# Kernel tuning notes

Hardware: AMD Instinct MI355X
Metric: run time of the kernel (lower is better)

## Reference

```python
import jax, jax.numpy as jnp
import numpy as np

N = 100_000   # nodes
E = 1_600_000 # edges
F = 64        # in_feats
H = 64        # hid
EPS = 1e-5


def setup_inputs() -> dict:
    key = jax.random.key(0)
    ks = jax.random.split(key, 12)
    s = 1.0 / np.sqrt(F)
    inp = {
        "x":   jax.random.normal(ks[0], (N, F), jnp.float32),
        "src": jax.random.randint(ks[1], (E,), 0, N, jnp.int32),
        "dst": jax.random.randint(ks[2], (E,), 0, N, jnp.int32),
        # GraphConv 1: in_feats -> hid
        "W1": jax.random.uniform(ks[3], (F, H), jnp.float32, -s, s),
        "b1": jnp.zeros((H,), jnp.float32),
        "g1": jnp.ones((H,), jnp.float32),
        "be1": jnp.zeros((H,), jnp.float32),
        # GraphConv 2: hid -> hid
        "W2": jax.random.uniform(ks[4], (H, H), jnp.float32, -s, s),
        "b2": jnp.zeros((H,), jnp.float32),
        "g2": jnp.ones((H,), jnp.float32),
        "be2": jnp.zeros((H,), jnp.float32),
        # classifier hid -> 2
        "Wc": jax.random.uniform(ks[5], (H, 2), jnp.float32, -s, s),
        "bc": jnp.zeros((2,), jnp.float32),
    }
    return inp


def _graph_conv(x, src, dst, W, b):
    # DGL GraphConv, norm='both', allow_zero_in_degree=True:
    # h = D_in^{-1/2} A (D_out^{-1/2} x) W + b, degrees clamped to >= 1.
    n = x.shape[0]
    ones = jnp.ones(src.shape[0], x.dtype)
    deg_out = jnp.clip(jax.ops.segment_sum(ones, src, num_segments=n), 1.0)
    deg_in = jnp.clip(jax.ops.segment_sum(ones, dst, num_segments=n), 1.0)
    h = x * jax.lax.rsqrt(deg_out)[:, None]
    m = jax.ops.segment_sum(h[src], dst, num_segments=n)  # gather-scatter SpMM
    m = m * jax.lax.rsqrt(deg_in)[:, None]
    return m @ W + b


def _bn(h, g, be):
    # BatchNorm1d training-mode math over nodes (biased variance).
    mu = h.mean(axis=0)
    var = h.var(axis=0)
    return (h - mu) * jax.lax.rsqrt(var + EPS) * g + be


def reference(x, src, dst, W1, b1, g1, be1, W2, b2, g2, be2, Wc, bc):
    h = jax.nn.relu(_bn(_graph_conv(x, src, dst, W1, b1), g1, be1))
    # dropout is identity in eval mode
    h = jax.nn.relu(_bn(_graph_conv(h, src, dst, W2, b2), g2, be2))
    hg = h.mean(axis=0, keepdims=True)  # [1, H] graph readout
    return hg @ Wc + bc                 # [1, 2]
```

## Files before the change

### kernel.cpp

```cpp
#include <hip/hip_runtime.h>
#include <hip/hip_fp16.h>

#define FDIM 64
#define EPS 1e-5f
#define NBUCK 1024
#define LOWB 7
#define LOWMASK 127
#define RB 256
#define RT 1024
#define GRP 16
#define NSLOT 8

typedef float v2f __attribute__((ext_vector_type(2)));

__global__ void k_hist(const int* __restrict__ src, const int* __restrict__ dst,
                       int* __restrict__ histS, int* __restrict__ histD, int E, int chunk) {
    __shared__ int hs[NBUCK], hd[NBUCK];
    int tid = threadIdx.x;
    hs[tid] = 0; hd[tid] = 0;
    __syncthreads();
    int b = blockIdx.x;
    int beg = b * chunk;
    int end = min(E, beg + chunk);
    int i = beg + tid * 4;
    for (; i + 3 < end; i += RT * 4) {
        int4 s = *(const int4*)(src + i);
        int4 d = *(const int4*)(dst + i);
        atomicAdd(&hs[s.x >> LOWB], 1); atomicAdd(&hd[d.x >> LOWB], 1);
        atomicAdd(&hs[s.y >> LOWB], 1); atomicAdd(&hd[d.y >> LOWB], 1);
        atomicAdd(&hs[s.z >> LOWB], 1); atomicAdd(&hd[d.z >> LOWB], 1);
        atomicAdd(&hs[s.w >> LOWB], 1); atomicAdd(&hd[d.w >> LOWB], 1);
    }
    if (i < end) {
        for (int j = i; j < end && j < i + 4; ++j) {
            atomicAdd(&hs[src[j] >> LOWB], 1);
            atomicAdd(&hd[dst[j] >> LOWB], 1);
        }
    }
    __syncthreads();
    histS[b * NBUCK + tid] = hs[tid];
    histD[b * NBUCK + tid] = hd[tid];
}

__global__ void k_scanA(const int* __restrict__ histS, const int* __restrict__ histD,
                        int* __restrict__ psumS, int* __restrict__ psumD) {
    int bid = blockIdx.x;
    int m = bid >> 6;
    int g = (bid >> 2) & (RB / GRP - 1);
    int c = bid & 3;
    const int* hist = m ? histD : histS;
    int* psum = m ? psumD : psumS;
    int k = c * 256 + threadIdx.x;
    int s = 0;
#pragma unroll
    for (int r = 0; r < GRP; ++r)
        s += hist[(g * GRP + r) * NBUCK + k];
    psum[g * NBUCK + k] = s;
}

__global__ void k_scanB(const int* __restrict__ psumS, int* __restrict__ baseS,
                        int* __restrict__ grpbaseS,
                        const int* __restrict__ psumD, int* __restrict__ baseD,
                        int* __restrict__ grpbaseD) {
    const int* psum = blockIdx.x ? psumD : psumS;
    int* base    = blockIdx.x ? baseD : baseS;
    int* grpbase = blockIdx.x ? grpbaseD : grpbaseS;
    __shared__ int s[NBUCK];
    int k = threadIdx.x;
    int ge[RB / GRP];
    int run = 0;
#pragma unroll
    for (int g = 0; g < RB / GRP; ++g) { ge[g] = run; run += psum[g * NBUCK + k]; }
    s[k] = run;
    __syncthreads();
    for (int off = 1; off < NBUCK; off <<= 1) {
        int t = (k >= off) ? s[k - off] : 0;
        __syncthreads();
        s[k] += t;
        __syncthreads();
    }
    int excl = (k > 0) ? s[k - 1] : 0;
    base[k] = excl;
    if (k == NBUCK - 1) base[NBUCK] = s[NBUCK - 1];
#pragma unroll
    for (int g = 0; g < RB / GRP; ++g)
        grpbase[g * NBUCK + k] = excl + ge[g];
}

__global__ void k_bucket(const int* __restrict__ src, const int* __restrict__ dst,
                         const int* __restrict__ histS, const int* __restrict__ histD,
                         const int* __restrict__ grpbaseS, const int* __restrict__ grpbaseD,
                         unsigned char* __restrict__ tmpS, int* __restrict__ tmpD,
                         int E, int chunk) {
    __shared__ int curS[NBUCK], curD[NBUCK];
    int tid = threadIdx.x;
    int b = blockIdx.x;
    int g = b / GRP;
    int rs = 0, rd = 0;
    for (int r = g * GRP; r < b; ++r) {
        rs += histS[r * NBUCK + tid];
        rd += histD[r * NBUCK + tid];
    }
    curS[tid] = grpbaseS[g * NBUCK + tid] + rs;
    curD[tid] = grpbaseD[g * NBUCK + tid] + rd;
    __syncthreads();
    int beg = b * chunk;
    int end = min(E, beg + chunk);
    int i = beg + tid * 4;
    for (; i + 3 < end; i += RT * 4) {
        int4 s = *(const int4*)(src + i);
        int4 d = *(const int4*)(dst + i);
        int p;
        p = atomicAdd(&curS[s.x >> LOWB], 1); tmpS[p] = (unsigned char)(s.x & LOWMASK);
        p = atomicAdd(&curS[s.y >> LOWB], 1); tmpS[p] = (unsigned char)(s.y & LOWMASK);
        p = atomicAdd(&curS[s.z >> LOWB], 1); tmpS[p] = (unsigned char)(s.z & LOWMASK);
        p = atomicAdd(&curS[s.w >> LOWB], 1); tmpS[p] = (unsigned char)(s.w & LOWMASK);
        p = atomicAdd(&curD[d.x >> LOWB], 1); tmpD[p] = (s.x << LOWB) | (d.x & LOWMASK);
        p = atomicAdd(&curD[d.y >> LOWB], 1); tmpD[p] = (s.y << LOWB) | (d.y & LOWMASK);
        p = atomicAdd(&curD[d.z >> LOWB], 1); tmpD[p] = (s.z << LOWB) | (d.z & LOWMASK);
        p = atomicAdd(&curD[d.w >> LOWB], 1); tmpD[p] = (s.w << LOWB) | (d.w & LOWMASK);
    }
    if (i < end) {
        for (int j = i; j < end && j < i + 4; ++j) {
            int sv = src[j], dv = dst[j];
            int p = atomicAdd(&curS[sv >> LOWB], 1);
            tmpS[p] = (unsigned char)(sv & LOWMASK);
            p = atomicAdd(&curD[dv >> LOWB], 1);
            tmpD[p] = (sv << LOWB) | (dv & LOWMASK);
        }
    }
}

__global__ void k_fine(const int* __restrict__ tmpD, const int* __restrict__ baseD,
                       int* __restrict__ csr_src, int* __restrict__ rowptr,
                       const unsigned char* __restrict__ tmpS, const int* __restrict__ baseS,
                       int* __restrict__ degO, const float* __restrict__ x,
                       unsigned char* __restrict__ buf8, int N, int nbuck) {
    __shared__ int hist[128];
    __shared__ int scanv[128];
    int tid = threadIdx.x;
    if (blockIdx.x < nbuck) {
        int b = blockIdx.x;
        int s0 = baseD[b];
        int s1 = baseD[b + 1];
        if (tid < 128) hist[tid] = 0;
        __syncthreads();
        for (int i = s0 + tid; i < s1; i += 256)
            atomicAdd(&hist[tmpD[i] & LOWMASK], 1);
        __syncthreads();
        int mine = (tid < 128) ? hist[tid] : 0;
        if (tid < 128) scanv[tid] = mine;
        __syncthreads();
        for (int off = 1; off < 128; off <<= 1) {
            int t = (tid < 128 && tid >= off) ? scanv[tid - off] : 0;
            __syncthreads();
            if (tid < 128) scanv[tid] += t;
            __syncthreads();
        }
        if (tid < 128) {
            int excl = scanv[tid] - mine;
            int d = (b << LOWB) + tid;
            if (d <= N) rowptr[d] = s0 + excl;
            hist[tid] = excl;
        }
        __syncthreads();
        for (int i = s0 + tid; i < s1; i += 256) {
            int p = tmpD[i];
            int pos = atomicAdd(&hist[p & LOWMASK], 1);
            csr_src[s0 + pos] = p >> LOWB;
        }
    } else {
        int b = blockIdx.x - nbuck;
        int s0 = baseS[b];
        int s1 = baseS[b + 1];
        if (tid < 128) hist[tid] = 0;
        __syncthreads();
        for (int i = s0 + tid; i < s1; i += 256)
            atomicAdd(&hist[tmpS[i]], 1);
        __syncthreads();
        if (tid < 128) {
            int d = (b << LOWB) + tid;
            if (d < N) degO[d] = hist[tid];
        }
        int node = (b << LOWB) + (tid >> 1);
        if (node < N) {
            float rs = rsqrtf((float)max(hist[tid >> 1], 1));
            int part = tid & 1;
            const float4* xr = (const float4*)(x + (size_t)node * FDIM) + part * 8;
            int4* orow = (int4*)(buf8 + (size_t)node * FDIM + part * 32);
            int wbuf[8];
#pragma unroll
            for (int q = 0; q < 4; ++q) {
                float4 a = xr[2 * q];
                float4 c = xr[2 * q + 1];
                int t = __builtin_amdgcn_cvt_pk_fp8_f32(a.x * rs, a.y * rs, 0, false);
                t     = __builtin_amdgcn_cvt_pk_fp8_f32(a.z * rs, a.w * rs, t, true);
                wbuf[2 * q] = t;
                t = __builtin_amdgcn_cvt_pk_fp8_f32(c.x * rs, c.y * rs, 0, false);
                t = __builtin_amdgcn_cvt_pk_fp8_f32(c.z * rs, c.w * rs, t, true);
                wbuf[2 * q + 1] = t;
            }
            orow[0] = make_int4(wbuf[0], wbuf[1], wbuf[2], wbuf[3]);
            orow[1] = make_int4(wbuf[4], wbuf[5], wbuf[6], wbuf[7]);
        }
    }
}

__global__ void k_spmm8(const unsigned char* __restrict__ hin, const int* __restrict__ rowptr,
                        const int* __restrict__ csr_src, __half* __restrict__ out, int N) {
    int wid = (blockIdx.x * blockDim.x + threadIdx.x) >> 6;
    int lane = threadIdx.x & 63;
    int g = lane >> 3;
    int sl = lane & 7;
    int row = wid * 8 + g;
    bool rv = row < N;
    int start = rv ? rowptr[row] : 0;
    int end   = rv ? rowptr[row + 1] : 0;
    int deg = end - start;
    int md = deg;
    md = max(md, __shfl_xor(md, 8));
    md = max(md, __shfl_xor(md, 16));
    md = max(md, __shfl_xor(md, 32));
    float acc[8] = {0.f, 0.f, 0.f, 0.f, 0.f, 0.f, 0.f, 0.f};
    int safe = (deg > 0) ? end - 1 : 0;
    int a0 = start + sl;
    int idx_cur = csr_src[(a0 < end) ? a0 : safe];
    for (int it = 0; it < md; it += 8) {
        int idx_nxt = 0;
        if (it + 8 < md) {
            int a = start + it + 8 + sl;
            idx_nxt = csr_src[(a < end) ? a : safe];
        }
        uint2 r[8];
#pragma unroll
        for (int j = 0; j < 8; ++j) {
            int bidx = __shfl(idx_cur, (g << 3) + j);
            r[j] = ((const uint2*)(hin + ((size_t)bidx << 6)))[sl];
        }
        __builtin_amdgcn_sched_barrier(0);
#pragma unroll
        for (int j = 0; j < 8; ++j) {
            float w = (it + j < deg) ? 1.f : 0.f;
            v2f a0v = __builtin_amdgcn_cvt_pk_f32_fp8((int)r[j].x, false);
            v2f a1v = __builtin_amdgcn_cvt_pk_f32_fp8((int)r[j].x, true);
            v2f a2v = __builtin_amdgcn_cvt_pk_f32_fp8((int)r[j].y, false);
            v2f a3v = __builtin_amdgcn_cvt_pk_f32_fp8((int)r[j].y, true);
            acc[0] = fmaf(w, a0v.x, acc[0]); acc[1] = fmaf(w, a0v.y, acc[1]);
            acc[2] = fmaf(w, a1v.x, acc[2]); acc[3] = fmaf(w, a1v.y, acc[3]);
            acc[4] = fmaf(w, a2v.x, acc[4]); acc[5] = fmaf(w, a2v.y, acc[5]);
            acc[6] = fmaf(w, a3v.x, acc[6]); acc[7] = fmaf(w, a3v.y, acc[7]);
        }
        idx_cur = idx_nxt;
    }
    if (rv) {
        float rs = rsqrtf(fmaxf((float)deg, 1.0f));
        union { float4 f; __half2 h[4]; } o;
        o.h[0] = __floats2half2_rn(acc[0] * rs, acc[1] * rs);
        o.h[1] = __floats2half2_rn(acc[2] * rs, acc[3] * rs);
        o.h[2] = __floats2half2_rn(acc[4] * rs, acc[5] * rs);
        o.h[3] = __floats2half2_rn(acc[6] * rs, acc[7] * rs);
        ((float4*)(out + ((size_t)row << 6)))[sl] = o.f;
    }
}

__global__ void k_gemm_reg(const __half* __restrict__ m, const float* __restrict__ W,
                           const float* __restrict__ b, __half* __restrict__ out, int N) {
    int n = blockIdx.x * blockDim.x + threadIdx.x;
    if (n >= N) return;
    const __half2* mrow = (const __half2*)(m + (size_t)n * FDIM);
    float acc[FDIM];
#pragma unroll
    for (int j = 0; j < FDIM; ++j) acc[j] = b[j];
    for (int k0 = 0; k0 < FDIM; k0 += 8) {
        float2 f0 = __half22float2(mrow[(k0 >> 1) + 0]);
        float2 f1 = __half22float2(mrow[(k0 >> 1) + 1]);
        float2 f2 = __half22float2(mrow[(k0 >> 1) + 2]);
        float2 f3 = __half22float2(mrow[(k0 >> 1) + 3]);
        float mreg[8] = {f0.x, f0.y, f1.x, f1.y, f2.x, f2.y, f3.x, f3.y};
#pragma unroll
        for (int k1 = 0; k1 < 8; ++k1) {
            const float* Wrow = W + (k0 + k1) * FDIM;
#pragma unroll
            for (int j = 0; j < FDIM; ++j)
                acc[j] = fmaf(mreg[k1], Wrow[j], acc[j]);
        }
    }
    float4* orow = (float4*)(out + (size_t)n * FDIM);
#pragma unroll
    for (int j = 0; j < FDIM; j += 8) {
        union { __half2 h[4]; float4 f; } u;
        u.h[0] = __floats2half2_rn(acc[j + 0], acc[j + 1]);
        u.h[1] = __floats2half2_rn(acc[j + 2], acc[j + 3]);
        u.h[2] = __floats2half2_rn(acc[j + 4], acc[j + 5]);
        u.h[3] = __floats2half2_rn(acc[j + 6], acc[j + 7]);
        orow[j >> 3] = u.f;
    }
}

__global__ void k_stats_fin(const __half* __restrict__ h, float* __restrict__ ssum,
                            float* __restrict__ ssq, const float* __restrict__ g,
                            float* __restrict__ mu, float* __restrict__ coef,
                            int* __restrict__ cnt, int N) {
    __shared__ float red[4][128];
    __shared__ int lastv;
    int tid = threadIdx.x;
    int sl = tid & 7;
    int nl = tid >> 3;
    float s[8] = {0.f,0.f,0.f,0.f,0.f,0.f,0.f,0.f};
    float q[8] = {0.f,0.f,0.f,0.f,0.f,0.f,0.f,0.f};
    int stride = gridDim.x * 32;
    for (int n = blockIdx.x * 32 + nl; n < N; n += stride) {
        union { float4 f; __half2 hh[4]; } u;
        u.f = ((const float4*)(h + ((size_t)n << 6)))[sl];
#pragma unroll
        for (int p = 0; p < 4; ++p) {
            float2 v = __half22float2(u.hh[p]);
            s[2*p]   += v.x; q[2*p]   += v.x * v.x;
            s[2*p+1] += v.y; q[2*p+1] += v.y * v.y;
        }
    }
#pragma unroll
    for (int off = 8; off < 64; off <<= 1) {
#pragma unroll
        for (int p = 0; p < 8; ++p) {
            s[p] += __shfl_xor(s[p], off);
            q[p] += __shfl_xor(q[p], off);
        }
    }
    int wv = tid >> 6, lane = tid & 63;
    if (lane < 8) {
#pragma unroll
        for (int p = 0; p < 8; ++p) {
            red[wv][lane * 8 + p] = s[p];
            red[wv][64 + lane * 8 + p] = q[p];
        }
    }
    __syncthreads();
    int slot = (blockIdx.x & (NSLOT - 1)) << 6;
    if (tid < 128) {
        float v = red[0][tid] + red[1][tid] + red[2][tid] + red[3][tid];
        if (tid < 64) atomicAdd(&ssum[slot + tid], v);
        else          atomicAdd(&ssq[slot + tid - 64], v);
    }
    __syncthreads();
    if (tid == 0)
        lastv = (__hip_atomic_fetch_add(cnt, 1, __ATOMIC_ACQ_REL,
                                        __HIP_MEMORY_SCOPE_AGENT) == (int)gridDim.x - 1);
    __syncthreads();
    if (lastv && tid < 64) {
        float sv = 0.f, qv = 0.f;
#pragma unroll
        for (int p = 0; p < NSLOT; ++p) {
            sv += __hip_atomic_load(&ssum[(p << 6) + tid], __ATOMIC_RELAXED,
                                    __HIP_MEMORY_SCOPE_AGENT);
            qv += __hip_atomic_load(&ssq[(p << 6) + tid], __ATOMIC_RELAXED,
                                    __HIP_MEMORY_SCOPE_AGENT);
        }
        float m = sv / (float)N;
        float var = qv / (float)N - m * m;
        mu[tid] = m;
        coef[tid] = rsqrtf(var + EPS) * g[tid];
    }
}

__global__ void k_bnrelu_scale(const float2* __restrict__ h, const float* __restrict__ mu,
                               const float* __restrict__ coef, const float* __restrict__ be,
                               const int* __restrict__ degO, int* __restrict__ out8, int n4) {
    int i = blockIdx.x * blockDim.x + threadIdx.x;
    if (i < n4) {
        int n = i >> 4;
        int j4 = (i & 15) << 2;
        float rs = rsqrtf((float)max(degO[n], 1));
        union { __half2 hh[2]; float2 f; } u;
        u.f = h[i];
        float2 v0 = __half22float2(u.hh[0]);
        float2 v1 = __half22float2(u.hh[1]);
        float r0 = fmaxf((v0.x - mu[j4 + 0]) * coef[j4 + 0] + be[j4 + 0], 0.f) * rs;
        float r1 = fmaxf((v0.y - mu[j4 + 1]) * coef[j4 + 1] + be[j4 + 1], 0.f) * rs;
        float r2 = fmaxf((v1.x - mu[j4 + 2]) * coef[j4 + 2] + be[j4 + 2], 0.f) * rs;
        float r3 = fmaxf((v1.y - mu[j4 + 3]) * coef[j4 + 3] + be[j4 + 3], 0.f) * rs;
        int wv = __builtin_amdgcn_cvt_pk_fp8_f32(r0, r1, 0, false);
        wv     = __builtin_amdgcn_cvt_pk_fp8_f32(r2, r3, wv, true);
        out8[i] = wv;
    }
}

__global__ void k_bnmean_fin(const __half* __restrict__ h, const float* __restrict__ mu,
                             const float* __restrict__ coef, const float* __restrict__ be,
                             float* __restrict__ hsum, const float* __restrict__ Wc,
                             const float* __restrict__ bc, float* __restrict__ out,
                             int* __restrict__ cnt, int N) {
    __shared__ float red[4][64];
    __shared__ float cls[128];
    __shared__ int lastv;
    int tid = threadIdx.x;
    int sl = tid & 7;
    int nl = tid >> 3;
    int j8 = sl * 8;
    float m_[8], c_[8], b_[8];
#pragma unroll
    for (int p = 0; p < 8; ++p) { m_[p] = mu[j8 + p]; c_[p] = coef[j8 + p]; b_[p] = be[j8 + p]; }
    float s[8] = {0.f,0.f,0.f,0.f,0.f,0.f,0.f,0.f};
    int stride = gridDim.x * 32;
    for (int n = blockIdx.x * 32 + nl; n < N; n += stride) {
        union { float4 f; __half2 hh[4]; } u;
        u.f = ((const float4*)(h + ((size_t)n << 6)))[sl];
#pragma unroll
        for (int p = 0; p < 4; ++p) {
            float2 v = __half22float2(u.hh[p]);
            s[2*p]   += fmaxf((v.x - m_[2*p])   * c_[2*p]   + b_[2*p],   0.f);
            s[2*p+1] += fmaxf((v.y - m_[2*p+1]) * c_[2*p+1] + b_[2*p+1], 0.f);
        }
    }
#pragma unroll
    for (int off = 8; off < 64; off <<= 1) {
#pragma unroll
        for (int p = 0; p < 8; ++p) s[p] += __shfl_xor(s[p], off);
    }
    int wv = tid >> 6, lane = tid & 63;
    if (lane < 8) {
#pragma unroll
        for (int p = 0; p < 8; ++p) red[wv][lane * 8 + p] = s[p];
    }
    __syncthreads();
    int slot = (blockIdx.x & (NSLOT - 1)) << 6;
    if (tid < 64)
        atomicAdd(&hsum[slot + tid], red[0][tid] + red[1][tid] + red[2][tid] + red[3][tid]);
    __syncthreads();
    if (tid == 0)
        lastv = (__hip_atomic_fetch_add(cnt, 1, __ATOMIC_ACQ_REL,
                                        __HIP_MEMORY_SCOPE_AGENT) == (int)gridDim.x - 1);
    __syncthreads();
    if (lastv) {
        if (tid < 64) {
            float hg = 0.f;
#pragma unroll
            for (int p = 0; p < NSLOT; ++p)
                hg += __hip_atomic_load(&hsum[(p << 6) + tid], __ATOMIC_RELAXED,
                                        __HIP_MEMORY_SCOPE_AGENT);
            hg /= (float)N;
            cls[tid]      = hg * Wc[tid * 2 + 0];
            cls[64 + tid] = hg * Wc[tid * 2 + 1];
        }
        __syncthreads();
        if (tid == 0) {
            float a = 0.f, bv = 0.f;
            for (int k = 0; k < 64; ++k) { a += cls[k]; bv += cls[64 + k]; }
            out[0] = a + bc[0];
            out[1] = bv + bc[1];
        }
    }
}

extern "C" void kernel_launch(void* const* d_in, const int* in_sizes, int n_in,
                              void* d_out, int out_size, void* d_ws, size_t ws_size,
                              hipStream_t stream) {
    const float* x   = (const float*)d_in[0];
    const int*   src = (const int*)d_in[1];
    const int*   dst = (const int*)d_in[2];
    const float* W1  = (const float*)d_in[3];
    const float* b1  = (const float*)d_in[4];
    const float* g1  = (const float*)d_in[5];
    const float* be1 = (const float*)d_in[6];
    const float* W2  = (const float*)d_in[7];
    const float* b2  = (const float*)d_in[8];
    const float* g2  = (const float*)d_in[9];
    const float* be2 = (const float*)d_in[10];
    const float* Wc  = (const float*)d_in[11];
    const float* bc  = (const float*)d_in[12];
    float* out = (float*)d_out;

    const int N = in_sizes[0] / FDIM;
    const int E = in_sizes[1];

    char* w = (char*)d_ws;
    __half* bufA   = (__half*)w;
    __half* bufB   = bufA + (size_t)N * FDIM;
    int*   csr_src = (int*)(bufB + (size_t)N * FDIM);
    int*   degO    = csr_src + E;
    int*   rowptr  = degO + N;
    int*   histS   = rowptr + N + 2;
    int*   histD   = histS + RB * NBUCK;
    int*   baseS   = histD + RB * NBUCK;
    int*   baseD   = baseS + NBUCK + 1;
    int*   psumS   = baseD + NBUCK + 1;
    int*   psumD   = psumS + (RB / GRP) * NBUCK;
    int*   grpbaseS= psumD + (RB / GRP) * NBUCK;
    int*   grpbaseD= grpbaseS + (RB / GRP) * NBUCK;
    float* stats   = (float*)(grpbaseD + (RB / GRP) * NBUCK);
    unsigned char* tmpS = (unsigned char*)(stats + 4096);
    unsigned char* buf8 = tmpS + E;
    int*           tmpD = (int*)bufB;

    float* sum1  = stats + 0;
    float* sq1   = stats + 512;
    float* sum2  = stats + 1024;
    float* sq2   = stats + 1536;
    float* hsum  = stats + 2048;
    float* mu1   = stats + 2560;
    float* coef1 = stats + 2624;
    float* mu2   = stats + 2688;
    float* coef2 = stats + 2752;
    int*   cnt1  = (int*)(stats + 2816);
    int*   cnt2  = (int*)(stats + 2817);
    int*   cnt3  = (int*)(stats + 2818);

    const int n4 = N * (FDIM / 4);
    const int spmm8_blocks = ((N + 7) / 8 + 3) / 4;
    const int nbuck_active = (N + LOWMASK) >> LOWB;
    const int chunk = ((E + RB - 1) / RB + 3) & ~3;

    hipMemsetAsync(stats, 0, 4096 * 4, stream);

    k_hist<<<RB, RT, 0, stream>>>(src, dst, histS, histD, E, chunk);
    k_scanA<<<2 * (RB / GRP) * 4, 256, 0, stream>>>(histS, histD, psumS, psumD);
    k_scanB<<<2, NBUCK, 0, stream>>>(psumS, baseS, grpbaseS, psumD, baseD, grpbaseD);
    k_bucket<<<RB, RT, 0, stream>>>(src, dst, histS, histD, grpbaseS, grpbaseD,
                                    tmpS, tmpD, E, chunk);
    k_fine<<<2 * nbuck_active, 256, 0, stream>>>(tmpD, baseD, csr_src, rowptr,
                                                 tmpS, baseS, degO, x, buf8, N, nbuck_active);

    k_spmm8<<<spmm8_blocks, 256, 0, stream>>>(buf8, rowptr, csr_src, bufB, N);
    k_gemm_reg<<<(N + 63) / 64, 64, 0, stream>>>(bufB, W1, b1, bufA, N);
    k_stats_fin<<<256, 256, 0, stream>>>(bufA, sum1, sq1, g1, mu1, coef1, cnt1, N);
    k_bnrelu_scale<<<(n4 + 255) / 256, 256, 0, stream>>>((const float2*)bufA, mu1, coef1, be1,
                                                         degO, (int*)buf8, n4);
    k_spmm8<<<spmm8_blocks, 256, 0, stream>>>(buf8, rowptr, csr_src, bufB, N);
    k_gemm_reg<<<(N + 63) / 64, 64, 0, stream>>>(bufB, W2, b2, bufA, N);
    k_stats_fin<<<256, 256, 0, stream>>>(bufA, sum2, sq2, g2, mu2, coef2, cnt2, N);
    k_bnmean_fin<<<256, 256, 0, stream>>>(bufA, mu2, coef2, be2, hsum, Wc, bc, out, cnt3, N);
}
```

Measured before the change: 282.5 us.

## Fuse BN statistics into GEMM and widen SpMM gathers to 16-byte loads

The BatchNorm sum and sum-of-squares reduction moves into the per-node GEMM kernel. A 64x65 shared-memory transpose gives per-column partial sums, which are added atomically into slots, and the last block finalizes mean and coefficient. This removes a separate stats kernel and a full re-read of the hidden activations. The SpMM kernel now gathers each neighbour row with 16-byte loads: each lane handles 16 features from alternating edges, and the two halves are combined with a shuffle. This halves the number of gather instructions but doubles accumulator registers. It also adds 1563 grid-wide atomics per layer instead of 256, and moves the stats reduction onto a 64-thread-block kernel.

```diff
diff --git a/kernel.cpp b/kernel.cpp
--- a/kernel.cpp
+++ b/kernel.cpp
@@ -210,8 +210,10 @@
                         const int* __restrict__ csr_src, __half* __restrict__ out, int N) {
     int wid = (blockIdx.x * blockDim.x + threadIdx.x) >> 6;
     int lane = threadIdx.x & 63;
-    int g = lane >> 3;
+    int g  = lane >> 3;
     int sl = lane & 7;
+    int e  = (lane >> 2) & 1;
+    int s  = lane & 3;
     int row = wid * 8 + g;
     bool rv = row < N;
     int start = rv ? rowptr[row] : 0;
@@ -221,7 +223,9 @@
     md = max(md, __shfl_xor(md, 8));
     md = max(md, __shfl_xor(md, 16));
     md = max(md, __shfl_xor(md, 32));
-    float acc[8] = {0.f, 0.f, 0.f, 0.f, 0.f, 0.f, 0.f, 0.f};
+    float acc[16];
+#pragma unroll
+    for (int q = 0; q < 16; ++q) acc[q] = 0.f;
     int safe = (deg > 0) ? end - 1 : 0;
     int a0 = start + sl;
     int idx_cur = csr_src[(a0 < end) ? a0 : safe];
@@ -231,43 +235,77 @@
             int a = start + it + 8 + sl;
             idx_nxt = csr_src[(a < end) ? a : safe];
         }
-        uint2 r[8];
-#pragma unroll
-        for (int j = 0; j < 8; ++j) {
-            int bidx = __shfl(idx_cur, (g << 3) + j);
-            r[j] = ((const uint2*)(hin + ((size_t)bidx << 6)))[sl];
-        }
+        int b0 = __shfl(idx_cur, (g << 3) + e);
+        int b1 = __shfl(idx_cur, (g << 3) + e + 2);
+        int b2 = __shfl(idx_cur, (g << 3) + e + 4);
+        int b3 = __shfl(idx_cur, (g << 3) + e + 6);
+        uint4 r0 = ((const uint4*)(hin + ((size_t)b0 << 6)))[s];
+        uint4 r1 = ((const uint4*)(hin + ((size_t)b1 << 6)))[s];
+        uint4 r2 = ((const uint4*)(hin + ((size_t)b2 << 6)))[s];
+        uint4 r3 = ((const uint4*)(hin + ((size_t)b3 << 6)))[s];
         __builtin_amdgcn_sched_barrier(0);
-#pragma unroll
-        for (int j = 0; j < 8; ++j) {
-            float w = (it + j < deg) ? 1.f : 0.f;
-            v2f a0v = __builtin_amdgcn_cvt_pk_f32_fp8((int)r[j].x, false);
-            v2f a1v = __builtin_amdgcn_cvt_pk_f32_fp8((int)r[j].x, true);
-            v2f a2v = __builtin_amdgcn_cvt_pk_f32_fp8((int)r[j].y, false);
-            v2f a3v = __builtin_amdgcn_cvt_pk_f32_fp8((int)r[j].y, true);
-            acc[0] = fmaf(w, a0v.x, acc[0]); acc[1] = fmaf(w, a0v.y, acc[1]);
-            acc[2] = fmaf(w, a1v.x, acc[2]); acc[3] = fmaf(w, a1v.y, acc[3]);
-            acc[4] = fmaf(w, a2v.x, acc[4]); acc[5] = fmaf(w, a2v.y, acc[5]);
-            acc[6] = fmaf(w, a3v.x, acc[6]); acc[7] = fmaf(w, a3v.y, acc[7]);
-        }
+        float w0 = (it + e     < deg) ? 1.f : 0.f;
+        float w1 = (it + e + 2 < deg) ? 1.f : 0.f;
+        float w2 = (it + e + 4 < deg) ? 1.f : 0.f;
+        float w3 = (it + e + 6 < deg) ? 1.f : 0.f;
+#define ACC16(RV, W) do { \
+        v2f t0 = __builtin_amdgcn_cvt_pk_f32_fp8((int)RV.x, false); \
+        v2f t1 = __builtin_amdgcn_cvt_pk_f32_fp8((int)RV.x, true);  \
+        v2f t2 = __builtin_amdgcn_cvt_pk_f32_fp8((int)RV.y, false); \
+        v2f t3 = __builtin_amdgcn_cvt_pk_f32_fp8((int)RV.y, true);  \
+        v2f t4 = __builtin_amdgcn_cvt_pk_f32_fp8((int)RV.z, false); \
+        v2f t5 = __builtin_amdgcn_cvt_pk_f32_fp8((int)RV.z, true);  \
+        v2f t6 = __builtin_amdgcn_cvt_pk_f32_fp8((int)RV.w, false); \
+        v2f t7 = __builtin_amdgcn_cvt_pk_f32_fp8((int)RV.w, true);  \
+        acc[0]  = fmaf(W, t0.x, acc[0]);  acc[1]  = fmaf(W, t0.y, acc[1]);  \
+        acc[2]  = fmaf(W, t1.x, acc[2]);  acc[3]  = fmaf(W, t1.y, acc[3]);  \
+        acc[4]  = fmaf(W, t2.x, acc[4]);  acc[5]  = fmaf(W, t2.y, acc[5]);  \
+        acc[6]  = fmaf(W, t3.x, acc[6]);  acc[7]  = fmaf(W, t3.y, acc[7]);  \
+        acc[8]  = fmaf(W, t4.x, acc[8]);  acc[9]  = fmaf(W, t4.y, acc[9]);  \
+        acc[10] = fmaf(W, t5.x, acc[10]); acc[11] = fmaf(W, t5.y, acc[11]); \
+        acc[12] = fmaf(W, t6.x, acc[12]); acc[13] = fmaf(W, t6.y, acc[13]); \
+        acc[14] = fmaf(W, t7.x, acc[14]); acc[15] = fmaf(W, t7.y, acc[15]); \
+    } while (0)
+        ACC16(r0, w0);
+        ACC16(r1, w1);
+        ACC16(r2, w2);
+        ACC16(r3, w3);
+#undef ACC16
         idx_cur = idx_nxt;
     }
+#pragma unroll
+    for (int q = 0; q < 16; ++q) acc[q] += __shfl_xor(acc[q], 4);
     if (rv) {
         float rs = rsqrtf(fmaxf((float)deg, 1.0f));
+        float v0 = e ? acc[8]  : acc[0];
+        float v1 = e ? acc[9]  : acc[1];
+        float v2 = e ? acc[10] : acc[2];
+        float v3 = e ? acc[11] : acc[3];
+        float v4 = e ? acc[12] : acc[4];
+        float v5 = e ? acc[13] : acc[5];
+        float v6 = e ? acc[14] : acc[6];
+        float v7 = e ? acc[15] : acc[7];
         union { float4 f; __half2 h[4]; } o;
-        o.h[0] = __floats2half2_rn(acc[0] * rs, acc[1] * rs);
-        o.h[1] = __floats2half2_rn(acc[2] * rs, acc[3] * rs);
-        o.h[2] = __floats2half2_rn(acc[4] * rs, acc[5] * rs);
-        o.h[3] = __floats2half2_rn(acc[6] * rs, acc[7] * rs);
-        ((float4*)(out + ((size_t)row << 6)))[sl] = o.f;
-    }
-}
-
-__global__ void k_gemm_reg(const __half* __restrict__ m, const float* __restrict__ W,
-                           const float* __restrict__ b, __half* __restrict__ out, int N) {
-    int n = blockIdx.x * blockDim.x + threadIdx.x;
-    if (n >= N) return;
-    const __half2* mrow = (const __half2*)(m + (size_t)n * FDIM);
+        o.h[0] = __floats2half2_rn(v0 * rs, v1 * rs);
+        o.h[1] = __floats2half2_rn(v2 * rs, v3 * rs);
+        o.h[2] = __floats2half2_rn(v4 * rs, v5 * rs);
+        o.h[3] = __floats2half2_rn(v6 * rs, v7 * rs);
+        *(float4*)(out + ((size_t)row << 6) + (s << 4) + (e << 3)) = o.f;
+    }
+}
+
+__global__ void k_gemm_stats(const __half* __restrict__ m, const float* __restrict__ W,
+                             const float* __restrict__ b, __half* __restrict__ out,
+                             float* __restrict__ ssum, float* __restrict__ ssq,
+                             const float* __restrict__ g, float* __restrict__ mu,
+                             float* __restrict__ coef, int* __restrict__ cnt, int N) {
+    __shared__ float sh[64][65];
+    __shared__ int lastv;
+    int tid = threadIdx.x;
+    int n = blockIdx.x * 64 + tid;
+    bool nv = n < N;
+    int nc = nv ? n : N - 1;
+    const __half2* mrow = (const __half2*)(m + (size_t)nc * FDIM);
     float acc[FDIM];
 #pragma unroll
     for (int j = 0; j < FDIM; ++j) acc[j] = b[j];
@@ -285,80 +323,47 @@
                 acc[j] = fmaf(mreg[k1], Wrow[j], acc[j]);
         }
     }
-    float4* orow = (float4*)(out + (size_t)n * FDIM);
-#pragma unroll
-    for (int j = 0; j < FDIM; j += 8) {
-        union { __half2 h[4]; float4 f; } u;
-        u.h[0] = __floats2half2_rn(acc[j + 0], acc[j + 1]);
-        u.h[1] = __floats2half2_rn(acc[j + 2], acc[j + 3]);
-        u.h[2] = __floats2half2_rn(acc[j + 4], acc[j + 5]);
-        u.h[3] = __floats2half2_rn(acc[j + 6], acc[j + 7]);
-        orow[j >> 3] = u.f;
-    }
-}
-
-__global__ void k_stats_fin(const __half* __restrict__ h, float* __restrict__ ssum,
-                            float* __restrict__ ssq, const float* __restrict__ g,
-                            float* __restrict__ mu, float* __restrict__ coef,
-                            int* __restrict__ cnt, int N) {
-    __shared__ float red[4][128];
-    __shared__ int lastv;
-    int tid = threadIdx.x;
-    int sl = tid & 7;
-    int nl = tid >> 3;
-    float s[8] = {0.f,0.f,0.f,0.f,0.f,0.f,0.f,0.f};
-    float q[8] = {0.f,0.f,0.f,0.f,0.f,0.f,0.f,0.f};
-    int stride = gridDim.x * 32;
-    for (int n = blockIdx.x * 32 + nl; n < N; n += stride) {
-        union { float4 f; __half2 hh[4]; } u;
-        u.f = ((const float4*)(h + ((size_t)n << 6)))[sl];
-#pragma unroll
-        for (int p = 0; p < 4; ++p) {
-            float2 v = __half22float2(u.hh[p]);
-            s[2*p]   += v.x; q[2*p]   += v.x * v.x;
-            s[2*p+1] += v.y; q[2*p+1] += v.y * v.y;
-        }
-    }
-#pragma unroll
-    for (int off = 8; off < 64; off <<= 1) {
-#pragma unroll
-        for (int p = 0; p < 8; ++p) {
-            s[p] += __shfl_xor(s[p], off);
-            q[p] += __shfl_xor(q[p], off);
-        }
-    }
-    int wv = tid >> 6, lane = tid & 63;
-    if (lane < 8) {
-#pragma unroll
-        for (int p = 0; p < 8; ++p) {
-            red[wv][lane * 8 + p] = s[p];
-            red[wv][64 + lane * 8 + p] = q[p];
-        }
-    }
-    __syncthreads();
+    if (nv) {
+        float4* orow = (float4*)(out + (size_t)n * FDIM);
+#pragma unroll
+        for (int j = 0; j < FDIM; j += 8) {
+            union { __half2 h[4]; float4 f; } u;
+            u.h[0] = __floats2half2_rn(acc[j + 0], acc[j + 1]);
+            u.h[1] = __floats2half2_rn(acc[j + 2], acc[j + 3]);
+            u.h[2] = __floats2half2_rn(acc[j + 4], acc[j + 5]);
+            u.h[3] = __floats2half2_rn(acc[j + 6], acc[j + 7]);
+            orow[j >> 3] = u.f;
+        }
+    }
+#pragma unroll
+    for (int j = 0; j < FDIM; ++j) sh[tid][j] = nv ? acc[j] : 0.f;
+    __syncthreads();
+    float sv = 0.f, qv = 0.f;
+#pragma unroll
+    for (int t = 0; t < 64; ++t) {
+        float v = sh[t][tid];
+        sv += v; qv = fmaf(v, v, qv);
+    }
     int slot = (blockIdx.x & (NSLOT - 1)) << 6;
-    if (tid < 128) {
-        float v = red[0][tid] + red[1][tid] + red[2][tid] + red[3][tid];
-        if (tid < 64) atomicAdd(&ssum[slot + tid], v);
-        else          atomicAdd(&ssq[slot + tid - 64], v);
-    }
+    atomicAdd(&ssum[slot + tid], sv);
+    atomicAdd(&ssq[slot + tid], qv);
     __syncthreads();
     if (tid == 0)
         lastv = (__hip_atomic_fetch_add(cnt, 1, __ATOMIC_ACQ_REL,
                                         __HIP_MEMORY_SCOPE_AGENT) == (int)gridDim.x - 1);
     __syncthreads();
-    if (lastv && tid < 64) {
-        float sv = 0.f, qv = 0.f;
+    if (lastv) {
+        float s2 = 0.f, q2 = 0.f;
 #pragma unroll
         for (int p = 0; p < NSLOT; ++p) {
-            sv += __hip_atomic_load(&ssum[(p << 6) + tid], __ATOMIC_RELAXED,
+            s2 += __hip_atomic_load(&ssum[(p << 6) + tid], __ATOMIC_RELAXED,
                                     __HIP_MEMORY_SCOPE_AGENT);
-            qv += __hip_atomic_load(&ssq[(p << 6) + tid], __ATOMIC_RELAXED,
+            q2 += __hip_atomic_load(&ssq[(p << 6) + tid], __ATOMIC_RELAXED,
                                     __HIP_MEMORY_SCOPE_AGENT);
         }
-        float m = sv / (float)N;
-        float var = qv / (float)N - m * m;
-        mu[tid] = m;
+        float mm = s2 / (float)N;
+        float var = q2 / (float)N - mm * mm;
+        mu[tid] = mm;
         coef[tid] = rsqrtf(var + EPS) * g[tid];
     }
 }
@@ -507,6 +512,7 @@
 
     const int n4 = N * (FDIM / 4);
     const int spmm8_blocks = ((N + 7) / 8 + 3) / 4;
+    const int gemm_blocks = (N + 63) / 64;
     const int nbuck_active = (N + LOWMASK) >> LOWB;
     const int chunk = ((E + RB - 1) / RB + 3) & ~3;
 
@@ -521,12 +527,12 @@
                                                  tmpS, baseS, degO, x, buf8, N, nbuck_active);
 
     k_spmm8<<<spmm8_blocks, 256, 0, stream>>>(buf8, rowptr, csr_src, bufB, N);
-    k_gemm_reg<<<(N + 63) / 64, 64, 0, stream>>>(bufB, W1, b1, bufA, N);
-    k_stats_fin<<<256, 256, 0, stream>>>(bufA, sum1, sq1, g1, mu1, coef1, cnt1, N);
+    k_gemm_stats<<<gemm_blocks, 64, 0, stream>>>(bufB, W1, b1, bufA, sum1, sq1,
+                                                 g1, mu1, coef1, cnt1, N);
     k_bnrelu_scale<<<(n4 + 255) / 256, 256, 0, stream>>>((const float2*)bufA, mu1, coef1, be1,
                                                          degO, (int*)buf8, n4);
     k_spmm8<<<spmm8_blocks, 256, 0, stream>>>(buf8, rowptr, csr_src, bufB, N);
-    k_gemm_reg<<<(N + 63) / 64, 64, 0, stream>>>(bufB, W2, b2, bufA, N);
-    k_stats_fin<<<256, 256, 0, stream>>>(bufA, sum2, sq2, g2, mu2, coef2, cnt2, N);
+    k_gemm_stats<<<gemm_blocks, 64, 0, stream>>>(bufB, W2, b2, bufA, sum2, sq2,
+                                                 g2, mu2, coef2, cnt2, N);
     k_bnmean_fin<<<256, 256, 0, stream>>>(bufA, mu2, coef2, be2, hsum, Wc, bc, out, cnt3, N);
 }
```

Result: slower. 360.1 us (+27.5%).
